# Kernel tuning notes

Hardware: AMD Instinct MI355X
Metric: run time of the kernel (lower is better)

## Reference

```python
import jax, jax.numpy as jnp
import numpy as np

HIDDEN = 32

def setup_inputs() -> dict:
    key = jax.random.key(0)
    ks = jax.random.split(key, 12)
    S, B, I, H = 1024, 2048, 1, HIDDEN
    s = 1.0 / np.sqrt(H)
    inp = {
        "x": jax.random.normal(ks[0], (S, B, I), dtype=jnp.float32),
        "h": jax.random.normal(ks[1], (2, B, H), dtype=jnp.float32),
        # RNN layer 0
        "W_ih0": jax.random.uniform(ks[2], (H, I), minval=-s, maxval=s, dtype=jnp.float32),
        "W_hh0": jax.random.uniform(ks[3], (H, H), minval=-s, maxval=s, dtype=jnp.float32),
        "b_ih0": jax.random.uniform(ks[4], (H,), minval=-s, maxval=s, dtype=jnp.float32),
        "b_hh0": jax.random.uniform(ks[5], (H,), minval=-s, maxval=s, dtype=jnp.float32),
        # RNN layer 1
        "W_ih1": jax.random.uniform(ks[6], (H, H), minval=-s, maxval=s, dtype=jnp.float32),
        "W_hh1": jax.random.uniform(ks[7], (H, H), minval=-s, maxval=s, dtype=jnp.float32),
        "b_ih1": jax.random.uniform(ks[8], (H,), minval=-s, maxval=s, dtype=jnp.float32),
        "b_hh1": jax.random.uniform(ks[9], (H,), minval=-s, maxval=s, dtype=jnp.float32),
        # output Linear(32, 1)
        "W_out": jax.random.uniform(ks[10], (1, H), minval=-s, maxval=s, dtype=jnp.float32),
        "b_out": jax.random.uniform(ks[11], (1,), minval=-s, maxval=s, dtype=jnp.float32),
    }
    return inp

def reference(x, h, W_ih0, W_hh0, b_ih0, b_hh0, W_ih1, W_hh1, b_ih1, b_hh1, W_out, b_out):
    # 2-layer Elman RNN with relu, time-major input (seq, batch, in).
    h1_0, h2_0 = h[0], h[1]

    def step(carry, x_t):
        h1, h2 = carry
        # h1' = relu(x W_ih0^T + b_ih0 + h1 W_hh0^T + b_hh0)
        h1n = jax.nn.relu(x_t @ W_ih0.T + b_ih0 + h1 @ W_hh0.T + b_hh0)
        h2n = jax.nn.relu(h1n @ W_ih1.T + b_ih1 + h2 @ W_hh1.T + b_hh1)
        return (h1n, h2n), h2n

    (h1_f, h2_f), r_out = jax.lax.scan(step, (h1_0, h2_0), x)  # r_out: (S, B, H)
    h_state = jnp.stack([h1_f, h2_f], axis=0)                   # (2, B, H)
    # Per-timestep Linear in the original == one batched projection over last dim.
    outs = r_out @ W_out.T + b_out                              # (S, B, 1)
    return outs, h_state
```

## Files before the change

### kernel.cpp

```cpp
#include <hip/hip_runtime.h>

typedef __attribute__((ext_vector_type(8))) short s8v;
typedef __attribute__((ext_vector_type(4))) float f4;
typedef __attribute__((ext_vector_type(4))) unsigned u4v;

#define SEQ 1024
#define BATCH 2048
#define SLOT 4
#define NSLOT (SEQ / SLOT + 3)

__device__ __forceinline__ unsigned pack2(float a, float b) {
  unsigned r;
  asm("v_cvt_pk_bf16_f32 %0, %1, %2" : "=v"(r) : "v"(a), "v"(b));
  return r;
}

__device__ __forceinline__ f4 MF(const unsigned (&a)[4], const unsigned (&b)[4], f4 c) {
  union U { unsigned u[4]; s8v v; } A, B;
  A.u[0] = a[0]; A.u[1] = a[1]; A.u[2] = a[2]; A.u[3] = a[3];
  B.u[0] = b[0]; B.u[1] = b[1]; B.u[2] = b[2]; B.u[3] = b[3];
  return __builtin_amdgcn_mfma_f32_16x16x32_bf16(A.v, B.v, c, 0, 0, 0);
}


__device__ __forceinline__ void convh(f4 va, f4 vb, unsigned (&hi)[4]) {
  hi[0] = pack2(va[0], va[1]);
  hi[1] = pack2(va[2], va[3]);
  hi[2] = pack2(vb[0], vb[1]);
  hi[3] = pack2(vb[2], vb[3]);
}

__device__ __forceinline__ void loadAh(const float* W, int row, int g, unsigned (&hi)[4]) {
  const float* p = W + row * 32;
  f4 u = *(const f4*)(p + 4 * g);
  f4 v = *(const f4*)(p + 16 + 4 * g);
  hi[0] = pack2(u[0], u[1]);
  hi[1] = pack2(u[2], u[3]);
  hi[2] = pack2(v[0], v[1]);
  hi[3] = pack2(v[2], v[3]);
}

__global__ __launch_bounds__(256) void rnn_fused(
    const float* __restrict__ x,    const float* __restrict__ h0,
    const float* __restrict__ Wih0, const float* __restrict__ Whh0,
    const float* __restrict__ bih0, const float* __restrict__ bhh0,
    const float* __restrict__ Wih1, const float* __restrict__ Whh1,
    const float* __restrict__ bih1, const float* __restrict__ bhh1,
    const float* __restrict__ Wout, const float* __restrict__ boutp,
    float* __restrict__ out)
{
  const int tid  = threadIdx.x;
  const int wid  = tid >> 6;
  const int lane = tid & 63;
  const int c = lane & 15;
  const int g = lane >> 4;
  const int b = blockIdx.x * 16 + c;
  const unsigned li = (unsigned)lane * 4u;

  __shared__ unsigned LH1[2][SLOT][256];
  __shared__ float    LP [2][SLOT][2][256];
  __shared__ unsigned LB2[2][SLOT][256];

  const f4 z = {0.f, 0.f, 0.f, 0.f};
  float* hs = out + SEQ * BATCH;

  if (wid == 0) {
    unsigned W00h[4], W01h[4];
    loadAh(Whh0, c,      g, W00h);
    loadAh(Whh0, 16 + c, g, W01h);
    f4 wih0A, wih0B, b0A, b0B;
#pragma unroll
    for (int r = 0; r < 4; ++r) {
      int j0 = 4 * g + r, j1 = 16 + 4 * g + r;
      wih0A[r] = Wih0[j0];            wih0B[r] = Wih0[j1];
      b0A[r]   = bih0[j0] + bhh0[j0]; b0B[r]   = bih0[j1] + bhh0[j1];
    }
    unsigned B1h[4];
    {
      const float* p1 = h0 + b * 32;
      f4 u = *(const f4*)(p1 + 4 * g);
      f4 v = *(const f4*)(p1 + 16 + 4 * g);
      convh(u, v, B1h);
    }
    f4 v10 = z, v11 = z;
    float xc[SLOT];
#pragma unroll
    for (int j = 0; j < SLOT; ++j) xc[j] = x[j * BATCH + b];

#pragma unroll 1
    for (int m = 0; m < NSLOT; ++m) {
      if (m < SEQ / SLOT) {
        float xn[SLOT];
#pragma unroll
        for (int j = 0; j < SLOT; ++j) {
          int ti = SLOT * m + SLOT + j;
          xn[j] = x[(ti < SEQ ? ti : SEQ - 1) * BATCH + b];
        }
#pragma unroll
        for (int j = 0; j < SLOT; ++j) {
          float XV = xc[j];
          f4 c00, c01;
#pragma unroll
          for (int r = 0; r < 4; ++r) {
            c00[r] = fmaf(XV, wih0A[r], b0A[r]);
            c01[r] = fmaf(XV, wih0B[r], b0B[r]);
          }
          c00 = MF(W00h, B1h, c00);
          c01 = MF(W01h, B1h, c01);
#pragma unroll
          for (int r = 0; r < 4; ++r) {
            v10[r] = fmaxf(c00[r], 0.f);
            v11[r] = fmaxf(c01[r], 0.f);
          }
          convh(v10, v11, B1h);
          u4v wh = { B1h[0], B1h[1], B1h[2], B1h[3] };
          *(u4v*)&LH1[m & 1][j][li] = wh;
        }
#pragma unroll
        for (int j = 0; j < SLOT; ++j) xc[j] = xn[j];
      }
      __syncthreads();
    }
    *(f4*)(hs + b * 32 + 4 * g)      = v10;
    *(f4*)(hs + b * 32 + 16 + 4 * g) = v11;

  } else if (wid == 1) {
    unsigned WiH0[4], WiH1[4];
    loadAh(Wih1, c,      g, WiH0);
    loadAh(Wih1, 16 + c, g, WiH1);
    f4 b1A, b1B;
#pragma unroll
    for (int r = 0; r < 4; ++r) {
      int j0 = 4 * g + r, j1 = 16 + 4 * g + r;
      b1A[r] = bih1[j0] + bhh1[j0];
      b1B[r] = bih1[j1] + bhh1[j1];
    }

#pragma unroll 1
    for (int m = 0; m < NSLOT; ++m) {
      if (m >= 1 && m <= SEQ / SLOT) {
        int p = (m - 1) & 1;
        u4v fh[SLOT];
#pragma unroll
        for (int j = 0; j < SLOT; ++j)
          fh[j] = *(const u4v*)&LH1[p][j][li];
#pragma unroll
        for (int j = 0; j < SLOT; ++j) {
          unsigned B1h[4] = { fh[j][0], fh[j][1], fh[j][2], fh[j][3] };
          f4 P0 = MF(WiH0, B1h, b1A);
          f4 P1 = MF(WiH1, B1h, b1B);
          *(f4*)&LP[m & 1][j][0][li] = P0;
          *(f4*)&LP[m & 1][j][1][li] = P1;
        }
      }
      __syncthreads();
    }

  } else if (wid == 2) {
    unsigned WhH0[4], WhH1[4];
    loadAh(Whh1, c,      g, WhH0);
    loadAh(Whh1, 16 + c, g, WhH1);
    unsigned B2h[4];
    f4 v20 = z, v21 = z;
    {
      const float* p2 = h0 + BATCH * 32 + b * 32;
      f4 u = *(const f4*)(p2 + 4 * g);
      f4 v = *(const f4*)(p2 + 16 + 4 * g);
      convh(u, v, B2h);
      v20 = u; v21 = v;
    }

#pragma unroll 1
    for (int m = 0; m < NSLOT; ++m) {
      if (m >= 2 && m <= SEQ / SLOT + 1) {
        int p = (m - 1) & 1;
        f4 Pa[SLOT], Pb[SLOT];
#pragma unroll
        for (int j = 0; j < SLOT; ++j) {
          Pa[j] = *(const f4*)&LP[p][j][0][li];
          Pb[j] = *(const f4*)&LP[p][j][1][li];
        }
#pragma unroll
        for (int j = 0; j < SLOT; ++j) {
          f4 r0 = MF(WhH0, B2h, Pa[j]);
          f4 s0 = MF(WhH1, B2h, Pb[j]);
#pragma unroll
          for (int r = 0; r < 4; ++r) {
            v20[r] = fmaxf(r0[r], 0.f);
            v21[r] = fmaxf(s0[r], 0.f);
          }
          convh(v20, v21, B2h);
          u4v wh = { B2h[0], B2h[1], B2h[2], B2h[3] };
          *(u4v*)&LB2[m & 1][j][li] = wh;
        }
      }
      __syncthreads();
    }
    *(f4*)(hs + BATCH * 32 + b * 32 + 4 * g)      = v20;
    *(f4*)(hs + BATCH * 32 + b * 32 + 16 + 4 * g) = v21;

  } else {
    unsigned WOh[4];
    {
      f4 u = *(const f4*)(Wout + 4 * g);
      f4 v = *(const f4*)(Wout + 16 + 4 * g);
      convh(u, v, WOh);
    }
    const float bO = boutp[0];
    const f4 cb = { bO, bO, bO, bO };

#pragma unroll 1
    for (int m = 0; m < NSLOT; ++m) {
      if (m >= 3) {
        int p = (m - 1) & 1;
        u4v th[SLOT];
#pragma unroll
        for (int j = 0; j < SLOT; ++j)
          th[j] = *(const u4v*)&LB2[p][j][li];
#pragma unroll
        for (int j = 0; j < SLOT; ++j) {
          unsigned B2h[4] = { th[j][0], th[j][1], th[j][2], th[j][3] };
          f4 cO = MF(WOh, B2h, cb);
          int t = SLOT * (m - 3) + j;
          if (g == 0) out[t * BATCH + b] = cO[0];
        }
      }
      __syncthreads();
    }
  }
}

extern "C" void kernel_launch(void* const* d_in, const int* in_sizes, int n_in,
                              void* d_out, int out_size, void* d_ws, size_t ws_size,
                              hipStream_t stream) {
  rnn_fused<<<dim3(128), dim3(256), 0, stream>>>(
      (const float*)d_in[0],  (const float*)d_in[1],  (const float*)d_in[2],
      (const float*)d_in[3],  (const float*)d_in[4],  (const float*)d_in[5],
      (const float*)d_in[6],  (const float*)d_in[7],  (const float*)d_in[8],
      (const float*)d_in[9],  (const float*)d_in[10], (const float*)d_in[11],
      (float*)d_out);
}
```

Baseline: 143.1 us.

## Store layer-1 input projections as packed bf16 and double slot depth

The wave that computes the layer-1 input projections now rounds them to bf16 with an add-and-perm trick and stores them packed in LDS, halving that buffer. The layer-1 recurrent wave unpacks them back to fp32 by shifting and masking before using them as MFMA accumulator seeds. The freed LDS is used to raise SLOT from 4 to 8, so the four pipeline stages hit block-wide barriers half as often. The cost is extra rounding of the projection plus bias, which lowers accuracy slightly, and the pipeline fill and drain stages become longer.

```diff
diff --git a/kernel.cpp b/kernel.cpp
--- a/kernel.cpp
+++ b/kernel.cpp
@@ -6,13 +6,19 @@
 
 #define SEQ 1024
 #define BATCH 2048
-#define SLOT 4
+#define SLOT 8
 #define NSLOT (SEQ / SLOT + 3)
 
 __device__ __forceinline__ unsigned pack2(float a, float b) {
   unsigned r;
   asm("v_cvt_pk_bf16_f32 %0, %1, %2" : "=v"(r) : "v"(a), "v"(b));
   return r;
+}
+
+__device__ __forceinline__ unsigned permpack(float a, float b) {
+  unsigned au = __float_as_uint(a) + 0x8000u;
+  unsigned bu = __float_as_uint(b) + 0x8000u;
+  return __builtin_amdgcn_perm(bu, au, 0x07060302u);
 }
 
 __device__ __forceinline__ f4 MF(const unsigned (&a)[4], const unsigned (&b)[4], f4 c) {
@@ -58,7 +64,7 @@
   const unsigned li = (unsigned)lane * 4u;
 
   __shared__ unsigned LH1[2][SLOT][256];
-  __shared__ float    LP [2][SLOT][2][256];
+  __shared__ unsigned LPp[2][SLOT][256];
   __shared__ unsigned LB2[2][SLOT][256];
 
   const f4 z = {0.f, 0.f, 0.f, 0.f};
@@ -149,8 +155,9 @@
           unsigned B1h[4] = { fh[j][0], fh[j][1], fh[j][2], fh[j][3] };
           f4 P0 = MF(WiH0, B1h, b1A);
           f4 P1 = MF(WiH1, B1h, b1B);
-          *(f4*)&LP[m & 1][j][0][li] = P0;
-          *(f4*)&LP[m & 1][j][1][li] = P1;
+          u4v wp = { permpack(P0[0], P0[1]), permpack(P0[2], P0[3]),
+                     permpack(P1[0], P1[1]), permpack(P1[2], P1[3]) };
+          *(u4v*)&LPp[m & 1][j][li] = wp;
         }
       }
       __syncthreads();
@@ -174,16 +181,23 @@
     for (int m = 0; m < NSLOT; ++m) {
       if (m >= 2 && m <= SEQ / SLOT + 1) {
         int p = (m - 1) & 1;
-        f4 Pa[SLOT], Pb[SLOT];
-#pragma unroll
-        for (int j = 0; j < SLOT; ++j) {
-          Pa[j] = *(const f4*)&LP[p][j][0][li];
-          Pb[j] = *(const f4*)&LP[p][j][1][li];
-        }
-#pragma unroll
-        for (int j = 0; j < SLOT; ++j) {
-          f4 r0 = MF(WhH0, B2h, Pa[j]);
-          f4 s0 = MF(WhH1, B2h, Pb[j]);
+        u4v tw[SLOT];
+#pragma unroll
+        for (int j = 0; j < SLOT; ++j)
+          tw[j] = *(const u4v*)&LPp[p][j][li];
+#pragma unroll
+        for (int j = 0; j < SLOT; ++j) {
+          f4 Pa, Pb;
+          Pa[0] = __uint_as_float(tw[j][0] << 16);
+          Pa[1] = __uint_as_float(tw[j][0] & 0xffff0000u);
+          Pa[2] = __uint_as_float(tw[j][1] << 16);
+          Pa[3] = __uint_as_float(tw[j][1] & 0xffff0000u);
+          Pb[0] = __uint_as_float(tw[j][2] << 16);
+          Pb[1] = __uint_as_float(tw[j][2] & 0xffff0000u);
+          Pb[2] = __uint_as_float(tw[j][3] << 16);
+          Pb[3] = __uint_as_float(tw[j][3] & 0xffff0000u);
+          f4 r0 = MF(WhH0, B2h, Pa);
+          f4 s0 = MF(WhH1, B2h, Pb);
 #pragma unroll
           for (int r = 0; r < 4; ++r) {
             v20[r] = fmaxf(r0[r], 0.f);
```

After: 131.3 us. -8.2%, faster.
